# Optimization experiments

Hardware: AMD Instinct MI355X
Metric: run time of the kernel (lower is better)

The kernel has to match this reference:

```python
import jax, jax.numpy as jnp
import numpy as np

N_NODES = 100000
N_EDGES = 500000
H = 128
EPS = 1e-5


def _mlp(x, W1, b1, W2, b2, W3, b3, g, beta):
    # 3-layer MLP (ReLU) + final LayerNorm, matching build_mlp(..., lay_norm=True, n_layers=3)
    h = jax.nn.relu(x @ W1 + b1)
    h = jax.nn.relu(h @ W2 + b2)
    h = h @ W3 + b3
    mu = jnp.mean(h, axis=-1, keepdims=True)
    var = jnp.var(h, axis=-1, keepdims=True)
    return (h - mu) * jax.lax.rsqrt(var + EPS) * g + beta


def setup_inputs() -> dict:
    key = jax.random.key(0)
    ks = jax.random.split(key, 20)
    s = lambda fan_in: 1.0 / np.sqrt(fan_in)
    inp = {
        "x": jax.random.normal(ks[0], (N_NODES, H), dtype=jnp.float32),
        "edge_attr": jax.random.normal(ks[1], (N_EDGES, H), dtype=jnp.float32),
        "edge_index": jax.random.randint(ks[2], (2, N_EDGES), 0, N_NODES, dtype=jnp.int64),
        # Edge MLP: in = 3H
        "eW1": jax.random.normal(ks[3], (3 * H, H), dtype=jnp.float32) * s(3 * H),
        "eb1": jnp.zeros((H,), jnp.float32),
        "eW2": jax.random.normal(ks[4], (H, H), dtype=jnp.float32) * s(H),
        "eb2": jnp.zeros((H,), jnp.float32),
        "eW3": jax.random.normal(ks[5], (H, H), dtype=jnp.float32) * s(H),
        "eb3": jnp.zeros((H,), jnp.float32),
        "eg": jnp.ones((H,), jnp.float32),
        "ebeta": jnp.zeros((H,), jnp.float32),
        # Node MLP: in = 2H
        "nW1": jax.random.normal(ks[6], (2 * H, H), dtype=jnp.float32) * s(2 * H),
        "nb1": jnp.zeros((H,), jnp.float32),
        "nW2": jax.random.normal(ks[7], (H, H), dtype=jnp.float32) * s(H),
        "nb2": jnp.zeros((H,), jnp.float32),
        "nW3": jax.random.normal(ks[8], (H, H), dtype=jnp.float32) * s(H),
        "nb3": jnp.zeros((H,), jnp.float32),
        "ng": jnp.ones((H,), jnp.float32),
        "nbeta": jnp.zeros((H,), jnp.float32),
    }
    return inp


def reference(x, edge_attr, edge_index,
              eW1, eb1, eW2, eb2, eW3, eb3, eg, ebeta,
              nW1, nb1, nW2, nb2, nW3, nb3, ng, nbeta):
    senders = edge_index[0]
    receivers = edge_index[1]
    # EdgeBlock: gather src/dst node feats, concat with edge feats, MLP (3H -> H)
    e_in = jnp.concatenate([x[senders], x[receivers], edge_attr], axis=-1)
    e_new = _mlp(e_in, eW1, eb1, eW2, eb2, eW3, eb3, eg, ebeta)
    # NodeBlock: scatter-sum edge messages to receiver nodes, concat with node feats, MLP (2H -> H)
    agg = jax.ops.segment_sum(e_new, receivers, num_segments=N_NODES)
    n_in = jnp.concatenate([x, agg], axis=-1)
    x_new = _mlp(n_in, nW1, nb1, nW2, nb2, nW3, nb3, ng, nbeta)
    # Residual connections
    return (x + x_new, edge_attr + e_new)
```

## Files before the change

### kernel.cpp

```cpp
#include <hip/hip_runtime.h>

#define N_NODES 100000
#define N_EDGES 500000
#define H 128
#define EPS 1e-5f
#define NT_E 1954
#define NT_N 391
#define PGRID 256

typedef __attribute__((ext_vector_type(8))) short bf16x8;
typedef __attribute__((ext_vector_type(4))) float f32x4;

__device__ __forceinline__ unsigned short f2bf(float f) {
  unsigned int u = __builtin_bit_cast(unsigned int, f);
  u += 0x7FFFu + ((u >> 16) & 1u);
  return (unsigned short)(u >> 16);
}
__device__ __forceinline__ float bf2f(unsigned short u) {
  return __builtin_bit_cast(float, (unsigned)u << 16);
}

__device__ __forceinline__ int swz(int r, int k) {
  return r * 128 + (k ^ ((r & 7) << 3));
}

union PK8 { unsigned short u[8]; uint4 q; };

#define GLDS16(g, l)                                                        \
  __builtin_amdgcn_global_load_lds(                                         \
      (const __attribute__((address_space(1))) void*)(g),                   \
      (__attribute__((address_space(3))) void*)(l), 16, 0, 0)

__device__ __forceinline__ void gemm_regA(const bf16x8 a[4], const unsigned short* Wb,
                                          int m0, int kq, f32x4 acc[8]) {
  #pragma unroll
  for (int kk = 0; kk < 4; ++kk) {
    const int k0 = kk * 32 + kq * 8;
    #pragma unroll
    for (int tc = 0; tc < 8; ++tc) {
      bf16x8 b = *(const bf16x8*)&Wb[swz(tc * 16 + m0, k0)];
      acc[tc] = __builtin_amdgcn_mfma_f32_16x16x32_bf16(a[kk], b, acc[tc], 0, 0, 0);
    }
  }
}

__device__ __forceinline__ void gemm_ldsA(const unsigned short* Hb, int wrow,
                                          const unsigned short* Wb,
                                          int m0, int kq, f32x4 acc[8]) {
  #pragma unroll
  for (int kk = 0; kk < 4; ++kk) {
    const int k0 = kk * 32 + kq * 8;
    bf16x8 a = *(const bf16x8*)&Hb[swz(wrow + m0, k0)];
    #pragma unroll
    for (int tc = 0; tc < 8; ++tc) {
      bf16x8 b = *(const bf16x8*)&Wb[swz(tc * 16 + m0, k0)];
      acc[tc] = __builtin_amdgcn_mfma_f32_16x16x32_bf16(a, b, acc[tc], 0, 0, 0);
    }
  }
}

__device__ __forceinline__ void zero_acc(f32x4 acc[8]) {
  #pragma unroll
  for (int b = 0; b < 8; ++b) acc[b] = (f32x4){0.f, 0.f, 0.f, 0.f};
}

__device__ __forceinline__ void ln4(const f32x4 acc[8], float mu[4], float rv[4]) {
  float s[4] = {0, 0, 0, 0}, ss[4] = {0, 0, 0, 0};
  #pragma unroll
  for (int tc = 0; tc < 8; ++tc)
    #pragma unroll
    for (int i = 0; i < 4; ++i) {
      const float v = acc[tc][i];
      s[i] += v;
      ss[i] += v * v;
    }
  #pragma unroll
  for (int off = 1; off < 16; off <<= 1)
    #pragma unroll
    for (int i = 0; i < 4; ++i) {
      s[i] += __shfl_xor(s[i], off);
      ss[i] += __shfl_xor(ss[i], off);
    }
  #pragma unroll
  for (int i = 0; i < 4; ++i) {
    const float m = s[i] * (1.0f / 128.0f);
    const float var = ss[i] * (1.0f / 128.0f) - m * m;
    mu[i] = m;
    rv[i] = rsqrtf(var + EPS);
  }
}


struct WSrc { const float* p[9]; };

__global__ void wprep_kernel(WSrc wsrc, unsigned short* __restrict__ wimg) {
  const int id = blockIdx.x * 256 + threadIdx.x;
  const int m = id >> 14;
  const int r = id & 16383;
  const int n = r & 127;
  const int k = r >> 7;
  wimg[m * 16384 + swz(n, k)] = f2bf(wsrc.p[m][k * 128 + n]);
}


__global__ __launch_bounds__(512, 2) void px_kernel(
    const float* __restrict__ x, const unsigned short* __restrict__ wimg,
    const float* __restrict__ eb1, const float* __restrict__ nb1,
    unsigned short* __restrict__ pxs, unsigned short* __restrict__ pxr,
    unsigned short* __restrict__ pxn) {
  extern __shared__ unsigned short smem[];
  const int t = threadIdx.x;
  #pragma unroll
  for (int j = 0; j < 12; ++j)
    GLDS16((const char*)wimg + j * 8192 + t * 16, (char*)smem + j * 8192 + t * 16);
  __syncthreads();

  const int lane = t & 63;
  const int wtile = (t >> 6) * 16;
  const int m0 = lane & 15;
  const int kq = lane >> 4;
  const long n0 = (long)blockIdx.x * 128;

  long an = n0 + wtile + m0;
  if (an > N_NODES - 1) an = N_NODES - 1;
  const float* px_ = x + an * H + kq * 8;
  bf16x8 aX[4];
  #pragma unroll
  for (int kk = 0; kk < 4; ++kk) {
    float4 v0 = *(const float4*)(px_ + kk * 32);
    float4 v1 = *(const float4*)(px_ + kk * 32 + 4);
    PK8 pk;
    pk.u[0] = f2bf(v0.x); pk.u[1] = f2bf(v0.y);
    pk.u[2] = f2bf(v0.z); pk.u[3] = f2bf(v0.w);
    pk.u[4] = f2bf(v1.x); pk.u[5] = f2bf(v1.y);
    pk.u[6] = f2bf(v1.z); pk.u[7] = f2bf(v1.w);
    aX[kk] = __builtin_bit_cast(bf16x8, pk.q);
  }
  const long cb = n0 + wtile + kq * 4;

  f32x4 acc[8];
  float bv[8];
  zero_acc(acc);
  gemm_regA(aX, smem, m0, kq, acc);
  #pragma unroll
  for (int tc = 0; tc < 8; ++tc) bv[tc] = eb1[tc * 16 + m0];
  #pragma unroll
  for (int i = 0; i < 4; ++i) {
    const long nn = cb + i;
    if (nn < N_NODES) {
      PK8 pk;
      #pragma unroll
      for (int tc = 0; tc < 8; ++tc) pk.u[tc] = f2bf(acc[tc][i] + bv[tc]);
      *(uint4*)(pxs + nn * H + m0 * 8) = pk.q;
    }
  }
  zero_acc(acc);
  gemm_regA(aX, smem + 16384, m0, kq, acc);
  #pragma unroll
  for (int i = 0; i < 4; ++i) {
    const long nn = cb + i;
    if (nn < N_NODES) {
      PK8 pk;
      #pragma unroll
      for (int tc = 0; tc < 8; ++tc) pk.u[tc] = f2bf(acc[tc][i]);
      *(uint4*)(pxr + nn * H + m0 * 8) = pk.q;
    }
  }
  zero_acc(acc);
  gemm_regA(aX, smem + 32768, m0, kq, acc);
  #pragma unroll
  for (int tc = 0; tc < 8; ++tc) bv[tc] = nb1[tc * 16 + m0];
  #pragma unroll
  for (int i = 0; i < 4; ++i) {
    const long nn = cb + i;
    if (nn < N_NODES) {
      PK8 pk;
      #pragma unroll
      for (int tc = 0; tc < 8; ++tc) pk.u[tc] = f2bf(acc[tc][i] + bv[tc]);
      *(uint4*)(pxn + nn * H + m0 * 8) = pk.q;
    }
  }
}


__global__ void hist_kernel(const int* __restrict__ ridx, unsigned* __restrict__ cnt) {
  const int e = blockIdx.x * 256 + threadIdx.x;
  if (e < N_EDGES) atomicAdd(&cnt[ridx[e]], 1u);
}

__global__ void scan1_kernel(const unsigned* __restrict__ cnt,
                             unsigned* __restrict__ offs,
                             unsigned* __restrict__ part) {
  __shared__ unsigned sh[256];
  const int t = threadIdx.x;
  const int base = blockIdx.x * 1024 + t * 4;
  unsigned v[4];
  #pragma unroll
  for (int i = 0; i < 4; ++i) v[i] = (base + i < N_NODES) ? cnt[base + i] : 0u;
  unsigned pre[4];
  pre[0] = 0; pre[1] = v[0]; pre[2] = v[0] + v[1]; pre[3] = pre[2] + v[2];
  const unsigned tot = pre[3] + v[3];
  sh[t] = tot;
  __syncthreads();
  for (int d = 1; d < 256; d <<= 1) {
    const unsigned u_ = (t >= d) ? sh[t - d] : 0u;
    __syncthreads();
    sh[t] += u_;
    __syncthreads();
  }
  const unsigned excl = sh[t] - tot;
  #pragma unroll
  for (int i = 0; i < 4; ++i)
    if (base + i < N_NODES) offs[base + i] = excl + pre[i];
  if (t == 255) part[blockIdx.x] = sh[255];
}

__global__ void scan2_kernel(unsigned* __restrict__ part, int n) {
  __shared__ unsigned sh[128];
  const int t = threadIdx.x;
  const unsigned v = (t < n) ? part[t] : 0u;
  sh[t] = v;
  __syncthreads();
  for (int d = 1; d < 128; d <<= 1) {
    const unsigned u_ = (t >= d) ? sh[t - d] : 0u;
    __syncthreads();
    sh[t] += u_;
    __syncthreads();
  }
  if (t < n) part[t] = sh[t] - v;
}

__global__ void scan3_kernel(unsigned* __restrict__ offs,
                             const unsigned* __restrict__ part,
                             unsigned* __restrict__ cursor) {
  const int i = blockIdx.x * 256 + threadIdx.x;
  if (i < N_NODES) {
    const unsigned o = offs[i] + part[i >> 10];
    offs[i] = o;
    cursor[i] = o;
  }
  if (i == 0) offs[N_NODES] = N_EDGES;
}

__global__ void scatter_kernel(const int* __restrict__ ridx,
                               unsigned* __restrict__ cursor,
                               int* __restrict__ slot) {
  const int e = blockIdx.x * 256 + threadIdx.x;
  if (e < N_EDGES) slot[e] = (int)atomicAdd(&cursor[ridx[e]], 1u);
}


__global__ __launch_bounds__(1024, 4) void edge_kernel(
    const float* __restrict__ edge_attr, const int* __restrict__ eidx,
    const int* __restrict__ slot, const unsigned short* __restrict__ wimg,
    const unsigned short* __restrict__ pxs, const unsigned short* __restrict__ pxr,
    const float* __restrict__ eb2, const float* __restrict__ eb3,
    const float* __restrict__ eg, const float* __restrict__ ebeta,
    float* __restrict__ out_e, unsigned short* __restrict__ enew) {
  extern __shared__ unsigned short smem[];
  unsigned short* Wc = smem;
  unsigned short* W2 = smem + 16384;
  unsigned short* W3 = smem + 32768;
  unsigned short* Hb = smem + 49152;
  const int t = threadIdx.x;
  #pragma unroll
  for (int j = 0; j < 6; ++j)
    GLDS16((const char*)(wimg + 3 * 16384) + j * 16384 + t * 16,
           (char*)smem + j * 16384 + t * 16);
  __syncthreads();

  const int lane = t & 63;
  const int wtile = (t >> 6) * 16;
  const int m0 = lane & 15;
  const int kq = lane >> 4;
  const int* sidx = eidx;
  const int* ridx = eidx + N_EDGES;

  for (int tile = blockIdx.x; tile < NT_E; tile += PGRID) {
    const long e0 = (long)tile * 256;
    const long cb = e0 + wtile + kq * 4;
    const long cbl = cb > (long)(N_EDGES - 4) ? (long)(N_EDGES - 4) : cb;
    int4 s4 = *(const int4*)&sidx[cbl];
    int4 r4 = *(const int4*)&ridx[cbl];
    int4 p4 = *(const int4*)&slot[cbl];
    const int* sp = (const int*)&s4;
    const int* rp = (const int*)&r4;
    const int* pp = (const int*)&p4;

    long ae = e0 + wtile + m0;
    if (ae > N_EDGES - 1) ae = N_EDGES - 1;
    const float* pe = edge_attr + ae * H + kq * 8;
    bf16x8 aE[4];
    #pragma unroll
    for (int kk = 0; kk < 4; ++kk) {
      float4 v0 = *(const float4*)(pe + kk * 32);
      float4 v1 = *(const float4*)(pe + kk * 32 + 4);
      PK8 pk;
      pk.u[0] = f2bf(v0.x); pk.u[1] = f2bf(v0.y);
      pk.u[2] = f2bf(v0.z); pk.u[3] = f2bf(v0.w);
      pk.u[4] = f2bf(v1.x); pk.u[5] = f2bf(v1.y);
      pk.u[6] = f2bf(v1.z); pk.u[7] = f2bf(v1.w);
      aE[kk] = __builtin_bit_cast(bf16x8, pk.q);
    }
    uint4 qs[4], qr[4];
    #pragma unroll
    for (int i = 0; i < 4; ++i) {
      qs[i] = *(const uint4*)(pxs + (long)sp[i] * H + m0 * 8);
      qr[i] = *(const uint4*)(pxr + (long)rp[i] * H + m0 * 8);
    }

    f32x4 acc[8];
    zero_acc(acc);
    gemm_regA(aE, Wc, m0, kq, acc);
    #pragma unroll
    for (int i = 0; i < 4; ++i) {
      const unsigned short* us = (const unsigned short*)&qs[i];
      const unsigned short* ur = (const unsigned short*)&qr[i];
      #pragma unroll
      for (int tc = 0; tc < 8; ++tc)
        acc[tc][i] += bf2f(us[tc]) + bf2f(ur[tc]);
    }
    #pragma unroll
    for (int tc = 0; tc < 8; ++tc) {
      const int col = tc * 16 + m0;
      #pragma unroll
      for (int i = 0; i < 4; ++i)
        Hb[swz(wtile + kq * 4 + i, col)] = f2bf(fmaxf(acc[tc][i], 0.f));
    }
    zero_acc(acc);
    gemm_ldsA(Hb, wtile, W2, m0, kq, acc);
    float b2v[8];
    #pragma unroll
    for (int tc = 0; tc < 8; ++tc) b2v[tc] = eb2[tc * 16 + m0];
    #pragma unroll
    for (int tc = 0; tc < 8; ++tc) {
      const int col = tc * 16 + m0;
      #pragma unroll
      for (int i = 0; i < 4; ++i)
        Hb[swz(wtile + kq * 4 + i, col)] = f2bf(fmaxf(acc[tc][i] + b2v[tc], 0.f));
    }
    zero_acc(acc);
    gemm_ldsA(Hb, wtile, W3, m0, kq, acc);

    float b3v[8], gv[8], btv[8];
    #pragma unroll
    for (int tc = 0; tc < 8; ++tc) {
      const int col = tc * 16 + m0;
      b3v[tc] = eb3[col];
      gv[tc] = eg[col];
      btv[tc] = ebeta[col];
    }
    #pragma unroll
    for (int tc = 0; tc < 8; ++tc)
      #pragma unroll
      for (int i = 0; i < 4; ++i) acc[tc][i] += b3v[tc];
    float mu[4], rv[4];
    ln4(acc, mu, rv);

    #pragma unroll
    for (int i = 0; i < 4; ++i) {
      const long er = cb + i;
      if (er < N_EDGES) {
        const long ps = (long)pp[i] * H;
        #pragma unroll
        for (int tc = 0; tc < 8; ++tc) {
          const int col = tc * 16 + m0;
          const float y = (acc[tc][i] - mu[i]) * rv[i] * gv[tc] + btv[tc];
          out_e[er * H + col] = edge_attr[er * H + col] + y;
          enew[ps + col] = f2bf(y);
        }
      }
    }
  }
}

__global__ __launch_bounds__(1024, 4) void node_kernel(
    const float* __restrict__ x, const unsigned short* __restrict__ enew,
    const unsigned* __restrict__ offs, const unsigned short* __restrict__ wimg,
    const unsigned short* __restrict__ pxn,
    const float* __restrict__ nb2, const float* __restrict__ nb3,
    const float* __restrict__ ng, const float* __restrict__ nbeta,
    float* __restrict__ out_x) {
  extern __shared__ unsigned short smem[];
  unsigned short* W1 = smem;
  unsigned short* W2 = smem + 16384;
  unsigned short* W3 = smem + 32768;
  unsigned short* Hb = smem + 49152;
  const int t = threadIdx.x;
  #pragma unroll
  for (int j = 0; j < 6; ++j)
    GLDS16((const char*)(wimg + 6 * 16384) + j * 16384 + t * 16,
           (char*)smem + j * 16384 + t * 16);
  __syncthreads();

  const int lane = t & 63;
  const int wtile = (t >> 6) * 16;
  const int m0 = lane & 15;
  const int kq = lane >> 4;

  for (int tile = blockIdx.x; tile < NT_N; tile += PGRID) {
    const long n0 = (long)tile * 256;
    long an = n0 + wtile + m0;
    if (an > N_NODES - 1) an = N_NODES - 1;
    const unsigned o0 = offs[an], o1 = offs[an + 1];

    float sm[4][8];
    #pragma unroll
    for (int kk = 0; kk < 4; ++kk)
      #pragma unroll
      for (int c = 0; c < 8; ++c) sm[kk][c] = 0.f;
    for (unsigned j = o0; j < o1; ++j) {
      const unsigned short* er = enew + (long)j * H + kq * 8;
      #pragma unroll
      for (int kk = 0; kk < 4; ++kk) {
        uint4 q = *(const uint4*)(er + kk * 32);
        const unsigned short* pu = (const unsigned short*)&q;
        #pragma unroll
        for (int c = 0; c < 8; ++c) sm[kk][c] += bf2f(pu[c]);
      }
    }
    bf16x8 aG[4];
    #pragma unroll
    for (int kk = 0; kk < 4; ++kk) {
      PK8 pk;
      #pragma unroll
      for (int c = 0; c < 8; ++c) pk.u[c] = f2bf(sm[kk][c]);
      aG[kk] = __builtin_bit_cast(bf16x8, pk.q);
    }

    const long cb = n0 + wtile + kq * 4;
    const long cbl = cb > (long)(N_NODES - 4) ? (long)(N_NODES - 4) : cb;
    uint4 qn[4];
    #pragma unroll
    for (int i = 0; i < 4; ++i)
      qn[i] = *(const uint4*)(pxn + (cbl + i) * H + m0 * 8);

    f32x4 acc[8];
    zero_acc(acc);
    gemm_regA(aG, W1, m0, kq, acc);
    #pragma unroll
    for (int i = 0; i < 4; ++i) {
      const unsigned short* un = (const unsigned short*)&qn[i];
      #pragma unroll
      for (int tc = 0; tc < 8; ++tc) acc[tc][i] += bf2f(un[tc]);
    }
    #pragma unroll
    for (int tc = 0; tc < 8; ++tc) {
      const int col = tc * 16 + m0;
      #pragma unroll
      for (int i = 0; i < 4; ++i)
        Hb[swz(wtile + kq * 4 + i, col)] = f2bf(fmaxf(acc[tc][i], 0.f));
    }
    zero_acc(acc);
    gemm_ldsA(Hb, wtile, W2, m0, kq, acc);
    float b2v[8];
    #pragma unroll
    for (int tc = 0; tc < 8; ++tc) b2v[tc] = nb2[tc * 16 + m0];
    #pragma unroll
    for (int tc = 0; tc < 8; ++tc) {
      const int col = tc * 16 + m0;
      #pragma unroll
      for (int i = 0; i < 4; ++i)
        Hb[swz(wtile + kq * 4 + i, col)] = f2bf(fmaxf(acc[tc][i] + b2v[tc], 0.f));
    }
    zero_acc(acc);
    gemm_ldsA(Hb, wtile, W3, m0, kq, acc);

    float b3v[8], gv[8], btv[8];
    #pragma unroll
    for (int tc = 0; tc < 8; ++tc) {
      const int col = tc * 16 + m0;
      b3v[tc] = nb3[col];
      gv[tc] = ng[col];
      btv[tc] = nbeta[col];
    }
    #pragma unroll
    for (int tc = 0; tc < 8; ++tc)
      #pragma unroll
      for (int i = 0; i < 4; ++i) acc[tc][i] += b3v[tc];
    float mu[4], rv[4];
    ln4(acc, mu, rv);

    #pragma unroll
    for (int i = 0; i < 4; ++i) {
      const long nn = cb + i;
      if (nn < N_NODES) {
        #pragma unroll
        for (int tc = 0; tc < 8; ++tc) {
          const int col = tc * 16 + m0;
          const float y = (acc[tc][i] - mu[i]) * rv[i] * gv[tc] + btv[tc];
          out_x[nn * H + col] = x[nn * H + col] + y;
        }
      }
    }
  }
}

extern "C" void kernel_launch(void* const* d_in, const int* in_sizes, int n_in,
                              void* d_out, int out_size, void* d_ws, size_t ws_size,
                              hipStream_t stream) {
  (void)in_sizes; (void)n_in; (void)out_size; (void)ws_size;
  const float* x         = (const float*)d_in[0];
  const float* edge_attr = (const float*)d_in[1];
  const int*   eidx      = (const int*)d_in[2];
  const float* eW1 = (const float*)d_in[3];
  const float* eb1 = (const float*)d_in[4];
  const float* eW2 = (const float*)d_in[5];
  const float* eb2 = (const float*)d_in[6];
  const float* eW3 = (const float*)d_in[7];
  const float* eb3 = (const float*)d_in[8];
  const float* eg  = (const float*)d_in[9];
  const float* ebt = (const float*)d_in[10];
  const float* nW1 = (const float*)d_in[11];
  const float* nb1 = (const float*)d_in[12];
  const float* nW2 = (const float*)d_in[13];
  const float* nb2 = (const float*)d_in[14];
  const float* nW3 = (const float*)d_in[15];
  const float* nb3 = (const float*)d_in[16];
  const float* ng  = (const float*)d_in[17];
  const float* nbt = (const float*)d_in[18];

  float* out_x = (float*)d_out;
  float* out_e = (float*)d_out + (size_t)N_NODES * H;

  char* w = (char*)d_ws;
  unsigned short* enew = (unsigned short*)(w + 0);
  unsigned short* pxs  = (unsigned short*)(w + 128000000);
  unsigned short* pxr  = (unsigned short*)(w + 153600000);
  unsigned short* pxn  = (unsigned short*)(w + 179200000);
  unsigned short* wimg = (unsigned short*)(w + 204800000);
  unsigned* offs   = (unsigned*)(w + 205094912);
  unsigned* cnt    = (unsigned*)(w + 205495040);
  unsigned* cursor = (unsigned*)(w + 205895168);
  unsigned* part   = (unsigned*)(w + 206295296);
  int* slot        = (int*)(w + 206296320);

  const int* ridx = eidx + N_EDGES;

  hipFuncSetAttribute((const void*)px_kernel,
                      hipFuncAttributeMaxDynamicSharedMemorySize, 98304);
  hipFuncSetAttribute((const void*)edge_kernel,
                      hipFuncAttributeMaxDynamicSharedMemorySize, 163840);
  hipFuncSetAttribute((const void*)node_kernel,
                      hipFuncAttributeMaxDynamicSharedMemorySize, 163840);

  hipMemsetAsync(cnt, 0, (size_t)N_NODES * sizeof(unsigned), stream);

  WSrc wsrc;
  wsrc.p[0] = eW1;
  wsrc.p[1] = eW1 + 16384;
  wsrc.p[2] = nW1;
  wsrc.p[3] = eW1 + 32768;
  wsrc.p[4] = eW2;
  wsrc.p[5] = eW3;
  wsrc.p[6] = nW1 + 16384;
  wsrc.p[7] = nW2;
  wsrc.p[8] = nW3;
  wprep_kernel<<<576, 256, 0, stream>>>(wsrc, wimg);

  px_kernel<<<(N_NODES + 127) / 128, 512, 98304, stream>>>(x, wimg, eb1, nb1,
                                                           pxs, pxr, pxn);

  hist_kernel<<<(N_EDGES + 255) / 256, 256, 0, stream>>>(ridx, cnt);
  scan1_kernel<<<(N_NODES + 1023) / 1024, 256, 0, stream>>>(cnt, offs, part);
  scan2_kernel<<<1, 128, 0, stream>>>(part, (N_NODES + 1023) / 1024);
  scan3_kernel<<<(N_NODES + 255) / 256, 256, 0, stream>>>(offs, part, cursor);
  scatter_kernel<<<(N_EDGES + 255) / 256, 256, 0, stream>>>(ridx, cursor, slot);

  edge_kernel<<<PGRID, 1024, 163840, stream>>>(edge_attr, eidx, slot, wimg,
                                               pxs, pxr, eb2, eb3, eg, ebt,
                                               out_e, enew);
  node_kernel<<<PGRID, 1024, 163840, stream>>>(x, enew, offs, wimg, pxn,
                                               nb2, nb3, ng, nbt, out_x);
}
```

Baseline: 495.7 us.

## Prefetch next edge tile and reuse staged edge_attr for the residual

The edge kernel now software-pipelines its tile loop. Sender/receiver indices and edge_attr rows for the next tile are loaded while the current tile runs its second and third GEMMs. The bf16-converted edge_attr is staged in LDS and repacked per lane, so the residual add no longer re-reads the fp32 edge_attr from global memory. This cuts a large stream of HBM traffic, but the residual output now uses bf16-rounded edge_attr, which lowers its precision. Bias, gamma and beta loads are hoisted out of both kernels' tile loops, and the MFMA loops are wrapped in s_setprio raises.

```diff
diff --git a/kernel.cpp b/kernel.cpp
--- a/kernel.cpp
+++ b/kernel.cpp
@@ -33,6 +33,7 @@
 
 __device__ __forceinline__ void gemm_regA(const bf16x8 a[4], const unsigned short* Wb,
                                           int m0, int kq, f32x4 acc[8]) {
+  __builtin_amdgcn_s_setprio(1);
   #pragma unroll
   for (int kk = 0; kk < 4; ++kk) {
     const int k0 = kk * 32 + kq * 8;
@@ -42,11 +43,13 @@
       acc[tc] = __builtin_amdgcn_mfma_f32_16x16x32_bf16(a[kk], b, acc[tc], 0, 0, 0);
     }
   }
+  __builtin_amdgcn_s_setprio(0);
 }
 
 __device__ __forceinline__ void gemm_ldsA(const unsigned short* Hb, int wrow,
                                           const unsigned short* Wb,
                                           int m0, int kq, f32x4 acc[8]) {
+  __builtin_amdgcn_s_setprio(1);
   #pragma unroll
   for (int kk = 0; kk < 4; ++kk) {
     const int k0 = kk * 32 + kq * 8;
@@ -57,6 +60,7 @@
       acc[tc] = __builtin_amdgcn_mfma_f32_16x16x32_bf16(a, b, acc[tc], 0, 0, 0);
     }
   }
+  __builtin_amdgcn_s_setprio(0);
 }
 
 __device__ __forceinline__ void zero_acc(f32x4 acc[8]) {
@@ -276,42 +280,85 @@
   const int* sidx = eidx;
   const int* ridx = eidx + N_EDGES;
 
-  for (int tile = blockIdx.x; tile < NT_E; tile += PGRID) {
-    const long e0 = (long)tile * 256;
-    const long cb = e0 + wtile + kq * 4;
-    const long cbl = cb > (long)(N_EDGES - 4) ? (long)(N_EDGES - 4) : cb;
-    int4 s4 = *(const int4*)&sidx[cbl];
-    int4 r4 = *(const int4*)&ridx[cbl];
-    int4 p4 = *(const int4*)&slot[cbl];
-    const int* sp = (const int*)&s4;
-    const int* rp = (const int*)&r4;
-    const int* pp = (const int*)&p4;
-
-    long ae = e0 + wtile + m0;
-    if (ae > N_EDGES - 1) ae = N_EDGES - 1;
-    const float* pe = edge_attr + ae * H + kq * 8;
-    bf16x8 aE[4];
-    #pragma unroll
-    for (int kk = 0; kk < 4; ++kk) {
-      float4 v0 = *(const float4*)(pe + kk * 32);
-      float4 v1 = *(const float4*)(pe + kk * 32 + 4);
-      PK8 pk;
-      pk.u[0] = f2bf(v0.x); pk.u[1] = f2bf(v0.y);
-      pk.u[2] = f2bf(v0.z); pk.u[3] = f2bf(v0.w);
-      pk.u[4] = f2bf(v1.x); pk.u[5] = f2bf(v1.y);
-      pk.u[6] = f2bf(v1.z); pk.u[7] = f2bf(v1.w);
-      aE[kk] = __builtin_bit_cast(bf16x8, pk.q);
-    }
+  float b2v[8], b3v[8], gv[8], btv[8];
+  #pragma unroll
+  for (int tc = 0; tc < 8; ++tc) {
+    const int col = tc * 16 + m0;
+    b2v[tc] = eb2[col];
+    b3v[tc] = eb3[col];
+    gv[tc] = eg[col];
+    btv[tc] = ebeta[col];
+  }
+
+  int tile = blockIdx.x;
+  long cbN, cblN;
+  int4 s4N, r4N;
+  float4 efN[8];
+
+#define EPRELOAD(T)                                                          \
+  {                                                                          \
+    const long e0_ = (long)(T) * 256;                                        \
+    cbN = e0_ + wtile + kq * 4;                                              \
+    cblN = cbN > (long)(N_EDGES - 4) ? (long)(N_EDGES - 4) : cbN;            \
+    s4N = *(const int4*)&sidx[cblN];                                         \
+    r4N = *(const int4*)&ridx[cblN];                                         \
+    long ae_ = e0_ + wtile + m0;                                             \
+    if (ae_ > N_EDGES - 1) ae_ = N_EDGES - 1;                                \
+    const float* pe_ = edge_attr + ae_ * H + kq * 8;                         \
+    _Pragma("unroll") for (int kk = 0; kk < 4; ++kk) {                       \
+      efN[2 * kk] = *(const float4*)(pe_ + kk * 32);                         \
+      efN[2 * kk + 1] = *(const float4*)(pe_ + kk * 32 + 4);                 \
+    }                                                                        \
+  }
+
+  EPRELOAD(tile);
+
+  for (;;) {
+    const long cb_c = cbN, cbl_c = cblN;
+    const int* sp = (const int*)&s4N;
+    const int* rp = (const int*)&r4N;
+
     uint4 qs[4], qr[4];
     #pragma unroll
     for (int i = 0; i < 4; ++i) {
       qs[i] = *(const uint4*)(pxs + (long)sp[i] * H + m0 * 8);
       qr[i] = *(const uint4*)(pxr + (long)rp[i] * H + m0 * 8);
     }
+
+    bf16x8 aE[4];
+    #pragma unroll
+    for (int kk = 0; kk < 4; ++kk) {
+      PK8 pk;
+      const float* v0 = (const float*)&efN[2 * kk];
+      const float* v1 = (const float*)&efN[2 * kk + 1];
+      #pragma unroll
+      for (int j = 0; j < 4; ++j) { pk.u[j] = f2bf(v0[j]); pk.u[4 + j] = f2bf(v1[j]); }
+      aE[kk] = __builtin_bit_cast(bf16x8, pk.q);
+    }
+
+    #pragma unroll
+    for (int kk = 0; kk < 4; ++kk)
+      *(uint4*)&Hb[swz(wtile + m0, kq * 8 + kk * 32)] = __builtin_bit_cast(uint4, aE[kk]);
 
     f32x4 acc[8];
     zero_acc(acc);
     gemm_regA(aE, Wc, m0, kq, acc);
+
+    unsigned eap_[16];
+    #pragma unroll
+    for (int i = 0; i < 4; ++i) {
+      const int r_ = wtile + kq * 4 + i;
+      #pragma unroll
+      for (int t2 = 0; t2 < 4; ++t2) {
+        unsigned lo = Hb[swz(r_, (2 * t2) * 16 + m0)];
+        unsigned hi = Hb[swz(r_, (2 * t2 + 1) * 16 + m0)];
+        eap_[i * 4 + t2] = lo | (hi << 16);
+      }
+    }
+
+    int4 p4 = *(const int4*)&slot[cbl_c];
+    const int* pp = (const int*)&p4;
+
     #pragma unroll
     for (int i = 0; i < 4; ++i) {
       const unsigned short* us = (const unsigned short*)&qs[i];
@@ -327,11 +374,13 @@
       for (int i = 0; i < 4; ++i)
         Hb[swz(wtile + kq * 4 + i, col)] = f2bf(fmaxf(acc[tc][i], 0.f));
     }
+
+    const int nt = tile + PGRID;
+    const bool more = nt < NT_E;
+    if (more) EPRELOAD(nt);
+
     zero_acc(acc);
     gemm_ldsA(Hb, wtile, W2, m0, kq, acc);
-    float b2v[8];
-    #pragma unroll
-    for (int tc = 0; tc < 8; ++tc) b2v[tc] = eb2[tc * 16 + m0];
     #pragma unroll
     for (int tc = 0; tc < 8; ++tc) {
       const int col = tc * 16 + m0;
@@ -342,14 +391,6 @@
     zero_acc(acc);
     gemm_ldsA(Hb, wtile, W3, m0, kq, acc);
 
-    float b3v[8], gv[8], btv[8];
-    #pragma unroll
-    for (int tc = 0; tc < 8; ++tc) {
-      const int col = tc * 16 + m0;
-      b3v[tc] = eb3[col];
-      gv[tc] = eg[col];
-      btv[tc] = ebeta[col];
-    }
     #pragma unroll
     for (int tc = 0; tc < 8; ++tc)
       #pragma unroll
@@ -359,19 +400,27 @@
 
     #pragma unroll
     for (int i = 0; i < 4; ++i) {
-      const long er = cb + i;
+      const long er = cb_c + i;
       if (er < N_EDGES) {
         const long ps = (long)pp[i] * H;
         #pragma unroll
-        for (int tc = 0; tc < 8; ++tc) {
-          const int col = tc * 16 + m0;
-          const float y = (acc[tc][i] - mu[i]) * rv[i] * gv[tc] + btv[tc];
-          out_e[er * H + col] = edge_attr[er * H + col] + y;
-          enew[ps + col] = f2bf(y);
+        for (int t2 = 0; t2 < 4; ++t2) {
+          const unsigned w_ = eap_[i * 4 + t2];
+          const int tcA = 2 * t2, tcB = 2 * t2 + 1;
+          const float yA = (acc[tcA][i] - mu[i]) * rv[i] * gv[tcA] + btv[tcA];
+          const float yB = (acc[tcB][i] - mu[i]) * rv[i] * gv[tcB] + btv[tcB];
+          out_e[er * H + tcA * 16 + m0] = bf2f((unsigned short)(w_ & 0xffffu)) + yA;
+          out_e[er * H + tcB * 16 + m0] = bf2f((unsigned short)(w_ >> 16)) + yB;
+          enew[ps + tcA * 16 + m0] = f2bf(yA);
+          enew[ps + tcB * 16 + m0] = f2bf(yB);
         }
       }
     }
-  }
+
+    if (!more) break;
+    tile = nt;
+  }
+#undef EPRELOAD
 }
 
 __global__ __launch_bounds__(1024, 4) void node_kernel(
@@ -398,6 +447,16 @@
   const int m0 = lane & 15;
   const int kq = lane >> 4;
 
+  float b2v[8], b3v[8], gv[8], btv[8];
+  #pragma unroll
+  for (int tc = 0; tc < 8; ++tc) {
+    const int col = tc * 16 + m0;
+    b2v[tc] = nb2[col];
+    b3v[tc] = nb3[col];
+    gv[tc] = ng[col];
+    btv[tc] = nbeta[col];
+  }
+
   for (int tile = blockIdx.x; tile < NT_N; tile += PGRID) {
     const long n0 = (long)tile * 256;
     long an = n0 + wtile + m0;
@@ -453,9 +512,6 @@
     }
     zero_acc(acc);
     gemm_ldsA(Hb, wtile, W2, m0, kq, acc);
-    float b2v[8];
-    #pragma unroll
-    for (int tc = 0; tc < 8; ++tc) b2v[tc] = nb2[tc * 16 + m0];
     #pragma unroll
     for (int tc = 0; tc < 8; ++tc) {
       const int col = tc * 16 + m0;
@@ -466,14 +522,6 @@
     zero_acc(acc);
     gemm_ldsA(Hb, wtile, W3, m0, kq, acc);
 
-    float b3v[8], gv[8], btv[8];
-    #pragma unroll
-    for (int tc = 0; tc < 8; ++tc) {
-      const int col = tc * 16 + m0;
-      b3v[tc] = nb3[col];
-      gv[tc] = ng[col];
-      btv[tc] = nbeta[col];
-    }
     #pragma unroll
     for (int tc = 0; tc < 8; ++tc)
       #pragma unroll
```

Result: slower. 849.9 us (+71.5%).
